# Kernel tuning notes

Hardware: AMD Instinct MI355X
Metric: run time of the kernel (lower is better)

The kernel has to match this reference:

```python
import jax, jax.numpy as jnp
import numpy as np

N_NODES = 100000
N_EDGES = 1000000
D_IN = 256
D_OUT = 64


def setup_inputs() -> dict:
    key = jax.random.key(0)
    k1, k2, k3, k4, k5, k6 = jax.random.split(key, 6)
    x = jax.random.normal(k1, (N_NODES, D_IN), dtype=jnp.float32)
    # Xavier-style uniform init: stdv = 1/sqrt(output_dim)
    stdv = 1.0 / np.sqrt(D_OUT)
    weight = jax.random.uniform(k2, (D_IN, D_OUT), dtype=jnp.float32, minval=-stdv, maxval=stdv)
    adj_vals = jax.random.uniform(k3, (N_EDGES,), dtype=jnp.float32)
    prelu_a = jnp.full((1,), 0.25, dtype=jnp.float32)  # nn.PReLU default
    row = jax.random.randint(k4, (N_EDGES,), 0, N_NODES, dtype=jnp.int32)
    col = jax.random.randint(k5, (N_EDGES,), 0, N_NODES, dtype=jnp.int32)
    return {"x": x, "weight": weight, "adj_vals": adj_vals, "prelu_a": prelu_a,
            "row": row, "col": col}


def reference(x, weight, adj_vals, prelu_a, row, col):
    # dense GEMM: [N, D_in] @ [D_in, D_out]
    hidden = x @ weight  # gc_drop=0 -> identity dropout
    # sparse adj spmm: out[i] = sum_{e: row[e]=i} adj_vals[e] * hidden[col[e]]
    msg = adj_vals[:, None] * hidden[col]  # [E, D_out]
    agg = jax.ops.segment_sum(msg, row, num_segments=N_NODES)  # [N, D_out]
    # PReLU with single shared slope
    out = jnp.where(agg > 0, agg, prelu_a * agg)
    return out
```

## Files before the change

kernel.cpp:

```cpp
#include <hip/hip_runtime.h>

#define N_NODES 100000
#define N_EDGES 1000000
#define D_IN    256
#define D_OUT   64

#define BKT_SHIFT   8
#define NODES_PER_B 256
#define N_BKT       391
#define BKT_CAP     3072
#define EPB         8192
#define BIN_BLOCKS  123
#define GEMM_BLOCKS 782

typedef __attribute__((ext_vector_type(8))) short short8;
typedef __attribute__((ext_vector_type(4))) float f32x4;

__device__ __forceinline__ unsigned short f2bf(float f) {
    unsigned int u = __float_as_uint(f);
    u = (u + 0x7fffu + ((u >> 16) & 1u)) >> 16;
    return (unsigned short)u;
}

__global__ __launch_bounds__(256) void gemm_bin_kernel(
    const float* __restrict__ x, const float* __restrict__ w,
    unsigned short* __restrict__ hiddenBf, int numTiles,
    const int* __restrict__ row, const int* __restrict__ col,
    const float* __restrict__ adj, int* __restrict__ gCursor,
    int2* __restrict__ edges)
{
    const int t = threadIdx.x;

    if (blockIdx.x < BIN_BLOCKS) {
        __shared__ int cnt[N_BKT];
        __shared__ int cbase[N_BKT];
        __shared__ int cur[N_BKT];

        const int e0 = blockIdx.x * EPB;

        for (int i = t; i < N_BKT; i += 256) cnt[i] = 0;
        __syncthreads();

        for (int i = t; i < EPB; i += 256) {
            int e = e0 + i;
            if (e < N_EDGES) atomicAdd(&cnt[row[e] >> BKT_SHIFT], 1);
        }
        __syncthreads();

        for (int i = t; i < N_BKT; i += 256) {
            int c = cnt[i];
            cbase[i] = c ? atomicAdd(&gCursor[i], c) : 0;
            cur[i] = 0;
        }
        __syncthreads();

        for (int i = t; i < EPB; i += 256) {
            int e = e0 + i;
            if (e < N_EDGES) {
                int r = row[e];
                int b = r >> BKT_SHIFT;
                int off = cbase[b] + atomicAdd(&cur[b], 1);
                if (off < BKT_CAP) {
                    edges[b * BKT_CAP + off] =
                        make_int2(((r & (NODES_PER_B - 1)) << 17) | col[e],
                                  __float_as_int(adj[e]));
                }
            }
        }
        return;
    }

    __shared__ unsigned short wT[64][264];

    for (int i = 0; i < 64; ++i) {
        int idx = t + i * 256;
        int k = idx >> 6, n = idx & 63;
        wT[n][k] = f2bf(w[idx]);
    }
    __syncthreads();

    const int lane = t & 63;
    const int wid  = t >> 6;
    const int n16  = lane & 15;
    const int quad = lane >> 4;

    const int waveGid   = (blockIdx.x - BIN_BLOCKS) * 4 + wid;
    const int waveCount = GEMM_BLOCKS * 4;

    for (int tile = waveGid; tile < numTiles; tile += waveCount) {
        const int r0 = tile * 16;
        const float* xrow = x + (size_t)(r0 + n16) * D_IN + quad * 8;

        short8 afrag[8];
#pragma unroll
        for (int kk = 0; kk < 8; ++kk) {
            float4 lo = *(const float4*)(xrow + kk * 32);
            float4 hi = *(const float4*)(xrow + kk * 32 + 4);
            short8 a;
            a[0] = (short)f2bf(lo.x); a[1] = (short)f2bf(lo.y);
            a[2] = (short)f2bf(lo.z); a[3] = (short)f2bf(lo.w);
            a[4] = (short)f2bf(hi.x); a[5] = (short)f2bf(hi.y);
            a[6] = (short)f2bf(hi.z); a[7] = (short)f2bf(hi.w);
            afrag[kk] = a;
        }

        f32x4 acc[4] = {{0.f,0.f,0.f,0.f},{0.f,0.f,0.f,0.f},
                        {0.f,0.f,0.f,0.f},{0.f,0.f,0.f,0.f}};
#pragma unroll
        for (int ct = 0; ct < 4; ++ct) {
#pragma unroll
            for (int kk = 0; kk < 8; ++kk) {
                short8 b = *(const short8*)&wT[ct * 16 + n16][kk * 32 + quad * 8];
                acc[ct] = __builtin_amdgcn_mfma_f32_16x16x32_bf16(
                    afrag[kk], b, acc[ct], 0, 0, 0);
            }
        }

#pragma unroll
        for (int ct = 0; ct < 4; ++ct)
#pragma unroll
            for (int reg = 0; reg < 4; ++reg)
                hiddenBf[(size_t)(r0 + quad * 4 + reg) * D_OUT + ct * 16 + n16]
                    = f2bf(acc[ct][reg]);
    }
}

__global__ __launch_bounds__(256) void csr_kernel(
    const int2* __restrict__ edges, const int* __restrict__ gCursor,
    int2* __restrict__ csr, unsigned int* __restrict__ startdeg)
{
    __shared__ int cnt[NODES_PER_B];
    __shared__ int cur[NODES_PER_B];

    const int b = blockIdx.x, t = threadIdx.x;
    cnt[t] = 0;
    __syncthreads();

    const int base = b * BKT_CAP;
    int size = gCursor[b];
    if (size > BKT_CAP) size = BKT_CAP;

    for (int i = t; i < size; i += 256)
        atomicAdd(&cnt[(unsigned)edges[base + i].x >> 17], 1);
    __syncthreads();

    int v = cnt[t];
    for (int off = 1; off < 256; off <<= 1) {
        int tmp = (t >= off) ? cnt[t - off] : 0;
        __syncthreads();
        cnt[t] += tmp;
        __syncthreads();
    }
    int gstart = base + cnt[t] - v;
    cur[t] = gstart;
    int node = b * NODES_PER_B + t;
    if (node < N_NODES)
        startdeg[node] = ((unsigned)gstart << 11) | (unsigned)(v < 2047 ? v : 2047);
    __syncthreads();

    for (int i = t; i < size; i += 256) {
        int2 rec = edges[base + i];
        int rl = (unsigned)rec.x >> 17;
        int pos = atomicAdd(&cur[rl], 1);
        csr[pos] = make_int2(rec.x & 0x1FFFF, rec.y);
    }
}

__global__ __launch_bounds__(256) void agg_kernel(
    const unsigned short* __restrict__ hiddenBf,
    const unsigned int* __restrict__ startdeg,
    const int2* __restrict__ csr, const float* __restrict__ prelu_a,
    float* __restrict__ out)
{
    const int wid  = threadIdx.x >> 6;
    const int lane = threadIdx.x & 63;
    const int node = blockIdx.x * 4 + wid;

    const unsigned int sd = startdeg[node];
    const int start = sd >> 11;
    const int deg   = sd & 2047;

    float acc = 0.f;
    for (int base = 0; base < deg; base += 64) {
        int take = deg - base;
        if (take > 64) take = 64;
        int2 rec = make_int2(0, 0);
        if (lane < take) rec = csr[start + base + lane];

        int j = 0;
        for (; j + 4 <= take; j += 4) {
            int c0 = __builtin_amdgcn_readlane(rec.x, j + 0);
            int c1 = __builtin_amdgcn_readlane(rec.x, j + 1);
            int c2 = __builtin_amdgcn_readlane(rec.x, j + 2);
            int c3 = __builtin_amdgcn_readlane(rec.x, j + 3);
            float v0 = __int_as_float(__builtin_amdgcn_readlane(rec.y, j + 0));
            float v1 = __int_as_float(__builtin_amdgcn_readlane(rec.y, j + 1));
            float v2 = __int_as_float(__builtin_amdgcn_readlane(rec.y, j + 2));
            float v3 = __int_as_float(__builtin_amdgcn_readlane(rec.y, j + 3));
            float h0 = __uint_as_float((unsigned)hiddenBf[(size_t)c0 * D_OUT + lane] << 16);
            float h1 = __uint_as_float((unsigned)hiddenBf[(size_t)c1 * D_OUT + lane] << 16);
            float h2 = __uint_as_float((unsigned)hiddenBf[(size_t)c2 * D_OUT + lane] << 16);
            float h3 = __uint_as_float((unsigned)hiddenBf[(size_t)c3 * D_OUT + lane] << 16);
            acc += v0 * h0;
            acc += v1 * h1;
            acc += v2 * h2;
            acc += v3 * h3;
        }
        for (; j < take; ++j) {
            int   c = __builtin_amdgcn_readlane(rec.x, j);
            float v = __int_as_float(__builtin_amdgcn_readlane(rec.y, j));
            float h = __uint_as_float((unsigned)hiddenBf[(size_t)c * D_OUT + lane] << 16);
            acc += v * h;
        }
    }
    const float a = prelu_a[0];
    out[(size_t)node * D_OUT + lane] = acc > 0.f ? acc : a * acc;
}

extern "C" void kernel_launch(void* const* d_in, const int* in_sizes, int n_in,
                              void* d_out, int out_size, void* d_ws, size_t ws_size,
                              hipStream_t stream)
{
    const float* x       = (const float*)d_in[0];
    const float* w       = (const float*)d_in[1];
    const float* adj     = (const float*)d_in[2];
    const float* prelu_a = (const float*)d_in[3];
    const int*   row     = (const int*)d_in[4];
    const int*   col     = (const int*)d_in[5];
    float* out = (float*)d_out;

    char* ws = (char*)d_ws;
    unsigned short* hiddenBf = (unsigned short*)(ws);
    int2*  edges    = (int2*)        (ws + 12800000);
    int2*  csr      = (int2*)        (ws + 22409216);
    unsigned int* startdeg = (unsigned int*)(ws + 32018944);
    int*   gCursor  = (int*)         (ws + 32419328);

    hipMemsetAsync(gCursor, 0, N_BKT * sizeof(int), stream);

    gemm_bin_kernel<<<BIN_BLOCKS + GEMM_BLOCKS, 256, 0, stream>>>(
        x, w, hiddenBf, (N_NODES + 15) / 16, row, col, adj, gCursor, edges);

    csr_kernel<<<N_BKT, 256, 0, stream>>>(edges, gCursor, csr, startdeg);

    agg_kernel<<<N_NODES / 4, 256, 0, stream>>>(hiddenBf, startdeg, csr, prelu_a, out);
}
```

Before: 255.8 us.

## Prefetch second GEMM tile, widen CSR blocks, unroll aggregation by eight

The GEMM path now gives each wave exactly two tiles and issues the loads for the second tile before running MFMA on the first, overlapping global x reads with compute. It also pads the LDS weight rows from 264 to 272 and adds a min-blocks-per-CU launch bound. The CSR kernel runs with 512 threads so edge scanning and scattering use twice as many threads. The aggregation loop is unrolled to eight gathers so more loads are in flight. The tradeoffs are higher register pressure from holding two tiles' worth of loads, and idle threads during the CSR scan.

Result: no change. 253.8 us (-0.8%).

```diff
diff --git a/kernel.cpp b/kernel.cpp
--- a/kernel.cpp
+++ b/kernel.cpp
@@ -12,6 +12,7 @@
 #define EPB         8192
 #define BIN_BLOCKS  123
 #define GEMM_BLOCKS 782
+#define NUM_TILES   6250
 
 typedef __attribute__((ext_vector_type(8))) short short8;
 typedef __attribute__((ext_vector_type(4))) float f32x4;
@@ -22,9 +23,32 @@
     return (unsigned short)u;
 }
 
-__global__ __launch_bounds__(256) void gemm_bin_kernel(
+__device__ __forceinline__ void mfma_store_tile(
+    const short8 afrag[8], const unsigned short wT[64][272],
+    unsigned short* __restrict__ hiddenBf, int r0, int n16, int quad)
+{
+    f32x4 acc[4] = {{0.f,0.f,0.f,0.f},{0.f,0.f,0.f,0.f},
+                    {0.f,0.f,0.f,0.f},{0.f,0.f,0.f,0.f}};
+#pragma unroll
+    for (int ct = 0; ct < 4; ++ct) {
+#pragma unroll
+        for (int kk = 0; kk < 8; ++kk) {
+            short8 b = *(const short8*)&wT[ct * 16 + n16][kk * 32 + quad * 8];
+            acc[ct] = __builtin_amdgcn_mfma_f32_16x16x32_bf16(
+                afrag[kk], b, acc[ct], 0, 0, 0);
+        }
+    }
+#pragma unroll
+    for (int ct = 0; ct < 4; ++ct)
+#pragma unroll
+        for (int reg = 0; reg < 4; ++reg)
+            hiddenBf[(size_t)(r0 + quad * 4 + reg) * D_OUT + ct * 16 + n16]
+                = f2bf(acc[ct][reg]);
+}
+
+__global__ __launch_bounds__(256, 2) void gemm_bin_kernel(
     const float* __restrict__ x, const float* __restrict__ w,
-    unsigned short* __restrict__ hiddenBf, int numTiles,
+    unsigned short* __restrict__ hiddenBf,
     const int* __restrict__ row, const int* __restrict__ col,
     const float* __restrict__ adj, int* __restrict__ gCursor,
     int2* __restrict__ edges)
@@ -70,7 +94,7 @@
         return;
     }
 
-    __shared__ unsigned short wT[64][264];
+    __shared__ unsigned short wT[64][272];
 
     for (int i = 0; i < 64; ++i) {
         int idx = t + i * 256;
@@ -84,48 +108,59 @@
     const int n16  = lane & 15;
     const int quad = lane >> 4;
 
-    const int waveGid   = (blockIdx.x - BIN_BLOCKS) * 4 + wid;
-    const int waveCount = GEMM_BLOCKS * 4;
-
-    for (int tile = waveGid; tile < numTiles; tile += waveCount) {
-        const int r0 = tile * 16;
-        const float* xrow = x + (size_t)(r0 + n16) * D_IN + quad * 8;
-
-        short8 afrag[8];
-#pragma unroll
-        for (int kk = 0; kk < 8; ++kk) {
-            float4 lo = *(const float4*)(xrow + kk * 32);
-            float4 hi = *(const float4*)(xrow + kk * 32 + 4);
+    const int waveGid = (blockIdx.x - BIN_BLOCKS) * 4 + wid;
+    const int t0 = waveGid * 2;
+    if (t0 >= NUM_TILES) return;
+
+    float4 lo[8], hi[8];
+    short8 afrag[8];
+
+    {
+        const float* xrow = x + (size_t)(t0 * 16 + n16) * D_IN + quad * 8;
+#pragma unroll
+        for (int kk = 0; kk < 8; ++kk) {
+            lo[kk] = *(const float4*)(xrow + kk * 32);
+            hi[kk] = *(const float4*)(xrow + kk * 32 + 4);
+        }
+    }
+#pragma unroll
+    for (int kk = 0; kk < 8; ++kk) {
+        short8 a;
+        a[0] = (short)f2bf(lo[kk].x); a[1] = (short)f2bf(lo[kk].y);
+        a[2] = (short)f2bf(lo[kk].z); a[3] = (short)f2bf(lo[kk].w);
+        a[4] = (short)f2bf(hi[kk].x); a[5] = (short)f2bf(hi[kk].y);
+        a[6] = (short)f2bf(hi[kk].z); a[7] = (short)f2bf(hi[kk].w);
+        afrag[kk] = a;
+    }
+
+    const int t1 = t0 + 1;
+    const bool have1 = t1 < NUM_TILES;
+    if (have1) {
+        const float* xrow = x + (size_t)(t1 * 16 + n16) * D_IN + quad * 8;
+#pragma unroll
+        for (int kk = 0; kk < 8; ++kk) {
+            lo[kk] = *(const float4*)(xrow + kk * 32);
+            hi[kk] = *(const float4*)(xrow + kk * 32 + 4);
+        }
+    }
+
+    mfma_store_tile(afrag, wT, hiddenBf, t0 * 16, n16, quad);
+
+    if (have1) {
+#pragma unroll
+        for (int kk = 0; kk < 8; ++kk) {
             short8 a;
-            a[0] = (short)f2bf(lo.x); a[1] = (short)f2bf(lo.y);
-            a[2] = (short)f2bf(lo.z); a[3] = (short)f2bf(lo.w);
-            a[4] = (short)f2bf(hi.x); a[5] = (short)f2bf(hi.y);
-            a[6] = (short)f2bf(hi.z); a[7] = (short)f2bf(hi.w);
+            a[0] = (short)f2bf(lo[kk].x); a[1] = (short)f2bf(lo[kk].y);
+            a[2] = (short)f2bf(lo[kk].z); a[3] = (short)f2bf(lo[kk].w);
+            a[4] = (short)f2bf(hi[kk].x); a[5] = (short)f2bf(hi[kk].y);
+            a[6] = (short)f2bf(hi[kk].z); a[7] = (short)f2bf(hi[kk].w);
             afrag[kk] = a;
         }
-
-        f32x4 acc[4] = {{0.f,0.f,0.f,0.f},{0.f,0.f,0.f,0.f},
-                        {0.f,0.f,0.f,0.f},{0.f,0.f,0.f,0.f}};
-#pragma unroll
-        for (int ct = 0; ct < 4; ++ct) {
-#pragma unroll
-            for (int kk = 0; kk < 8; ++kk) {
-                short8 b = *(const short8*)&wT[ct * 16 + n16][kk * 32 + quad * 8];
-                acc[ct] = __builtin_amdgcn_mfma_f32_16x16x32_bf16(
-                    afrag[kk], b, acc[ct], 0, 0, 0);
-            }
-        }
-
-#pragma unroll
-        for (int ct = 0; ct < 4; ++ct)
-#pragma unroll
-            for (int reg = 0; reg < 4; ++reg)
-                hiddenBf[(size_t)(r0 + quad * 4 + reg) * D_OUT + ct * 16 + n16]
-                    = f2bf(acc[ct][reg]);
-    }
-}
-
-__global__ __launch_bounds__(256) void csr_kernel(
+        mfma_store_tile(afrag, wT, hiddenBf, t1 * 16, n16, quad);
+    }
+}
+
+__global__ __launch_bounds__(512) void csr_kernel(
     const int2* __restrict__ edges, const int* __restrict__ gCursor,
     int2* __restrict__ csr, unsigned int* __restrict__ startdeg)
 {
@@ -133,32 +168,35 @@
     __shared__ int cur[NODES_PER_B];
 
     const int b = blockIdx.x, t = threadIdx.x;
-    cnt[t] = 0;
+    if (t < NODES_PER_B) cnt[t] = 0;
     __syncthreads();
 
     const int base = b * BKT_CAP;
     int size = gCursor[b];
     if (size > BKT_CAP) size = BKT_CAP;
 
-    for (int i = t; i < size; i += 256)
+    for (int i = t; i < size; i += 512)
         atomicAdd(&cnt[(unsigned)edges[base + i].x >> 17], 1);
     __syncthreads();
 
-    int v = cnt[t];
-    for (int off = 1; off < 256; off <<= 1) {
-        int tmp = (t >= off) ? cnt[t - off] : 0;
-        __syncthreads();
-        cnt[t] += tmp;
-        __syncthreads();
-    }
-    int gstart = base + cnt[t] - v;
-    cur[t] = gstart;
-    int node = b * NODES_PER_B + t;
-    if (node < N_NODES)
-        startdeg[node] = ((unsigned)gstart << 11) | (unsigned)(v < 2047 ? v : 2047);
-    __syncthreads();
-
-    for (int i = t; i < size; i += 256) {
+    int v = (t < NODES_PER_B) ? cnt[t] : 0;
+    for (int off = 1; off < NODES_PER_B; off <<= 1) {
+        int tmp = (t < NODES_PER_B && t >= off) ? cnt[t - off] : 0;
+        __syncthreads();
+        if (t < NODES_PER_B) cnt[t] += tmp;
+        __syncthreads();
+    }
+    if (t < NODES_PER_B) {
+        int gstart = base + cnt[t] - v;
+        cur[t] = gstart;
+        int node = b * NODES_PER_B + t;
+        if (node < N_NODES)
+            startdeg[node] = ((unsigned)gstart << 11) |
+                             (unsigned)(v < 2047 ? v : 2047);
+    }
+    __syncthreads();
+
+    for (int i = t; i < size; i += 512) {
         int2 rec = edges[base + i];
         int rl = (unsigned)rec.x >> 17;
         int pos = atomicAdd(&cur[rl], 1);
@@ -188,28 +226,25 @@
         if (lane < take) rec = csr[start + base + lane];
 
         int j = 0;
-        for (; j + 4 <= take; j += 4) {
-            int c0 = __builtin_amdgcn_readlane(rec.x, j + 0);
-            int c1 = __builtin_amdgcn_readlane(rec.x, j + 1);
-            int c2 = __builtin_amdgcn_readlane(rec.x, j + 2);
-            int c3 = __builtin_amdgcn_readlane(rec.x, j + 3);
-            float v0 = __int_as_float(__builtin_amdgcn_readlane(rec.y, j + 0));
-            float v1 = __int_as_float(__builtin_amdgcn_readlane(rec.y, j + 1));
-            float v2 = __int_as_float(__builtin_amdgcn_readlane(rec.y, j + 2));
-            float v3 = __int_as_float(__builtin_amdgcn_readlane(rec.y, j + 3));
-            float h0 = __uint_as_float((unsigned)hiddenBf[(size_t)c0 * D_OUT + lane] << 16);
-            float h1 = __uint_as_float((unsigned)hiddenBf[(size_t)c1 * D_OUT + lane] << 16);
-            float h2 = __uint_as_float((unsigned)hiddenBf[(size_t)c2 * D_OUT + lane] << 16);
-            float h3 = __uint_as_float((unsigned)hiddenBf[(size_t)c3 * D_OUT + lane] << 16);
-            acc += v0 * h0;
-            acc += v1 * h1;
-            acc += v2 * h2;
-            acc += v3 * h3;
+        for (; j + 8 <= take; j += 8) {
+            int   c[8]; float v[8]; float h[8];
+#pragma unroll
+            for (int u = 0; u < 8; ++u) {
+                c[u] = __builtin_amdgcn_readlane(rec.x, j + u);
+                v[u] = __int_as_float(__builtin_amdgcn_readlane(rec.y, j + u));
+            }
+#pragma unroll
+            for (int u = 0; u < 8; ++u)
+                h[u] = __uint_as_float(
+                    (unsigned)hiddenBf[(size_t)c[u] * D_OUT + lane] << 16);
+#pragma unroll
+            for (int u = 0; u < 8; ++u) acc += v[u] * h[u];
         }
         for (; j < take; ++j) {
             int   c = __builtin_amdgcn_readlane(rec.x, j);
             float v = __int_as_float(__builtin_amdgcn_readlane(rec.y, j));
-            float h = __uint_as_float((unsigned)hiddenBf[(size_t)c * D_OUT + lane] << 16);
+            float h = __uint_as_float(
+                (unsigned)hiddenBf[(size_t)c * D_OUT + lane] << 16);
             acc += v * h;
         }
     }
@@ -239,9 +274,9 @@
     hipMemsetAsync(gCursor, 0, N_BKT * sizeof(int), stream);
 
     gemm_bin_kernel<<<BIN_BLOCKS + GEMM_BLOCKS, 256, 0, stream>>>(
-        x, w, hiddenBf, (N_NODES + 15) / 16, row, col, adj, gCursor, edges);
-
-    csr_kernel<<<N_BKT, 256, 0, stream>>>(edges, gCursor, csr, startdeg);
+        x, w, hiddenBf, row, col, adj, gCursor, edges);
+
+    csr_kernel<<<N_BKT, 512, 0, stream>>>(edges, gCursor, csr, startdeg);
 
     agg_kernel<<<N_NODES / 4, 256, 0, stream>>>(hiddenBf, startdeg, csr, prelu_a, out);
 }
```
